# Optimization experiments

Measured on AMD Instinct MI355X. Metric: run time of the kernel, lower is better.

## Reference

```python
import jax, jax.numpy as jnp
import numpy as np

N_EMBED = 1024
N_HEAD = 16
D = N_EMBED // N_HEAD
B, T = 2, 2048
EPS = 1e-5


def _layer_norm(x, w, b):
    mu = jnp.mean(x, axis=-1, keepdims=True)
    var = jnp.mean(jnp.square(x - mu), axis=-1, keepdims=True)
    return (x - mu) * jax.lax.rsqrt(var + EPS) * w + b


def setup_inputs() -> dict:
    key = jax.random.key(0)
    ks = jax.random.split(key, 13)
    E = N_EMBED
    s_attn = 1.0 / np.sqrt(E)
    s_fc = 1.0 / np.sqrt(E)
    s_proj = 1.0 / np.sqrt(4 * E)
    return {
        "x": jax.random.normal(ks[0], (B, T, E), jnp.float32),
        "ln1_w": jnp.ones((E,), jnp.float32),
        "ln1_b": jnp.ones((E,), jnp.float32),
        "w_qkv": jax.random.normal(ks[1], (E, 3 * E), jnp.float32) * s_attn,
        "b_qkv": jax.random.normal(ks[2], (3 * E,), jnp.float32) * 0.02,
        "w_o": jax.random.normal(ks[3], (E, E), jnp.float32) * s_attn,
        "b_o": jax.random.normal(ks[4], (E,), jnp.float32) * 0.02,
        "ln2_w": jnp.ones((E,), jnp.float32),
        "ln2_b": jnp.ones((E,), jnp.float32),
        "w_fc": jax.random.normal(ks[5], (E, 4 * E), jnp.float32) * s_fc,
        "b_fc": jax.random.normal(ks[6], (4 * E,), jnp.float32) * 0.02,
        "w_proj": jax.random.normal(ks[7], (4 * E, E), jnp.float32) * s_proj,
        "b_proj": jax.random.normal(ks[8], (E,), jnp.float32) * 0.02,
    }


def reference(x, ln1_w, ln1_b, w_qkv, b_qkv, w_o, b_o, ln2_w, ln2_b, w_fc, b_fc, w_proj, b_proj):
    Bb, Tt, E = x.shape
    # --- attention branch ---
    h = _layer_norm(x, ln1_w, ln1_b)
    qkv = h @ w_qkv + b_qkv                         # [B,T,3E]
    q, k, v = jnp.split(qkv, 3, axis=-1)
    q = q.reshape(Bb, Tt, N_HEAD, D).transpose(0, 2, 1, 3)  # [B,H,T,D]
    k = k.reshape(Bb, Tt, N_HEAD, D).transpose(0, 2, 1, 3)
    v = v.reshape(Bb, Tt, N_HEAD, D).transpose(0, 2, 1, 3)
    scale = 1.0 / np.sqrt(D)
    a = scale * jnp.einsum("bhqd,bhkd->bhqk", q, k)  # [B,H,T,T]
    causal = jnp.tril(jnp.ones((Tt, Tt), bool))
    a = jnp.where(causal, a, -jnp.inf)
    a = jax.nn.softmax(a, axis=-1)
    y = jnp.einsum("bhqk,bhkd->bhqd", a, v)          # [B,H,T,D]
    y = y.transpose(0, 2, 1, 3).reshape(Bb, Tt, E)
    y = y @ w_o + b_o
    x = x + y
    # --- MLP branch ---
    h = _layer_norm(x, ln2_w, ln2_b)
    h = jax.nn.gelu(h @ w_fc + b_fc, approximate=False)
    h = h @ w_proj + b_proj
    return x + h
```

## Files before the change

### kernel.cpp

```cpp
#include <hip/hip_runtime.h>
#include <cstdint>
#include <cstddef>

#define E 1024
#define TT 2048
#define NB 2
#define NH 16
#define HD 64

using u16 = unsigned short;
using bf16x8 = __attribute__((ext_vector_type(8))) __bf16;
using floatx4 = __attribute__((ext_vector_type(4))) float;
using s16x4 = __attribute__((ext_vector_type(4))) short;

__device__ __forceinline__ float b2f(u16 u) {
  unsigned int x = ((unsigned int)u) << 16;
  float f;
  __builtin_memcpy(&f, &x, 4);
  return f;
}
__device__ __forceinline__ u16 f2b(float f) {
  unsigned int x;
  __builtin_memcpy(&x, &f, 4);
  x += 0x7fffu + ((x >> 16) & 1u);
  return (u16)(x >> 16);
}
__device__ __forceinline__ u16 f2b_fast(float f) {
  unsigned int x;
  float g = f * 1.001953125f;
  __builtin_memcpy(&x, &g, 4);
  return (u16)(x >> 16);
}

__device__ __forceinline__ void async16(const u16* g, u16* l) {
  __builtin_amdgcn_global_load_lds(
      (const __attribute__((address_space(1))) unsigned int*)g,
      (__attribute__((address_space(3))) unsigned int*)l, 16, 0, 0);
}

__device__ __forceinline__ floatx4 mfma32(bf16x8 a, bf16x8 b, floatx4 c) {
  return __builtin_amdgcn_mfma_f32_16x16x32_bf16(a, b, c, 0, 0, 0);
}

__device__ __forceinline__ floatx4 mfma16(s16x4 a, s16x4 b, floatx4 c) {
#if defined(__HIP_DEVICE_COMPILE__)
  return __builtin_amdgcn_mfma_f32_16x16x16bf16_1k(a, b, c, 0, 0, 0);
#else
  return c;
#endif
}

__global__ __launch_bounds__(256) void wconv_all(
    const float* __restrict__ w0, const float* __restrict__ w1,
    const float* __restrict__ w2, const float* __restrict__ w3,
    u16* __restrict__ o0, u16* __restrict__ o1, u16* __restrict__ o2,
    u16* __restrict__ o3) {
  __shared__ float tile[32][33];
  const int t = blockIdx.x;
  const float* w;
  u16* o;
  int K, N, nx, ti;
  if (t < 3072) { w = w0; o = o0; K = 1024; N = 3072; nx = 96; ti = t; }
  else if (t < 4096) { w = w1; o = o1; K = 1024; N = 1024; nx = 32; ti = t - 3072; }
  else if (t < 8192) { w = w2; o = o2; K = 1024; N = 4096; nx = 128; ti = t - 4096; }
  else { w = w3; o = o3; K = 4096; N = 1024; nx = 32; ti = t - 8192; }
  const int n0 = (ti % nx) * 32, k0 = (ti / nx) * 32;
  const int tx = threadIdx.x, ty = threadIdx.y;
#pragma unroll
  for (int i = 0; i < 32; i += 8)
    tile[ty + i][tx] = w[(size_t)(k0 + ty + i) * N + (n0 + tx)];
  __syncthreads();
#pragma unroll
  for (int i = 0; i < 32; i += 8)
    o[(size_t)(n0 + ty + i) * K + (k0 + tx)] = f2b(tile[tx][ty + i]);
}

__global__ __launch_bounds__(256) void ln_kernel(const float* __restrict__ x,
                                                 const float* __restrict__ w,
                                                 const float* __restrict__ bvec,
                                                 u16* __restrict__ outb) {
  const int row = blockIdx.x;
  const int t = threadIdx.x;
  const float4 v = ((const float4*)(x + (size_t)row * E))[t];
  float s1 = v.x + v.y + v.z + v.w;
  float s2 = v.x * v.x + v.y * v.y + v.z * v.z + v.w * v.w;
#pragma unroll
  for (int off = 32; off > 0; off >>= 1) {
    s1 += __shfl_down(s1, off);
    s2 += __shfl_down(s2, off);
  }
  __shared__ float r1[4], r2[4];
  if ((t & 63) == 0) { r1[t >> 6] = s1; r2[t >> 6] = s2; }
  __syncthreads();
  s1 = r1[0] + r1[1] + r1[2] + r1[3];
  s2 = r2[0] + r2[1] + r2[2] + r2[3];
  const float mean = s1 * (1.f / E);
  const float var = s2 * (1.f / E) - mean * mean;
  const float rstd = rsqrtf(var + 1e-5f);
  const float4 wv = ((const float4*)w)[t];
  const float4 bv = ((const float4*)bvec)[t];
  const u16 o0 = f2b((v.x - mean) * rstd * wv.x + bv.x);
  const u16 o1 = f2b((v.y - mean) * rstd * wv.y + bv.y);
  const u16 o2 = f2b((v.z - mean) * rstd * wv.z + bv.z);
  const u16 o3 = f2b((v.w - mean) * rstd * wv.w + bv.w);
  uint2 pk;
  pk.x = (unsigned)o0 | ((unsigned)o1 << 16);
  pk.y = (unsigned)o2 | ((unsigned)o3 << 16);
  ((uint2*)(outb + (size_t)row * E))[t] = pk;
}

template <int MODE, int ROWS>
__global__ __launch_bounds__(512) void gemm_bt(const u16* __restrict__ A,
                                               const u16* __restrict__ BT,
                                               const float* __restrict__ bias,
                                               const float* __restrict__ res,
                                               void* __restrict__ outp,
                                               int M, int N, int K) {
  constexpr int NJ = (ROWS == 256) ? 4 : 2;
  __shared__ __align__(16) u16 As[2][ROWS * 32];
  __shared__ __align__(16) u16 Bs[2][128 * 32];
  const int tid = threadIdx.x;
  const int wave = tid >> 6, lane = tid & 63;

  const int gx = gridDim.x, gy = gridDim.y;
  const int L = blockIdx.y * gx + blockIdx.x;
  const int xc = L & 7, wi = L >> 3;
  const int cpg = gx >> 2;
  const int rpg = gy >> 1;
  const int bxs = (xc >> 1) * cpg + (wi % cpg);
  const int bys = (xc & 1) * rpg + (wi / cpg);

  const int row0 = bys * ROWS, col0 = bxs * 128;
  const int wm = (ROWS == 256) ? (wave & 3) * 64 : (wave & 1) * 64;
  const int wn = (ROWS == 256) ? (wave >> 2) * 64 : (wave >> 1) * 32;
  const int r = lane & 15, qd = lane >> 4;

  floatx4 acc[4][NJ];
#pragma unroll
  for (int i = 0; i < 4; i++)
#pragma unroll
    for (int j = 0; j < NJ; j++) acc[i][j] = (floatx4){0.f, 0.f, 0.f, 0.f};

  const int cA0 = tid, cA1 = tid + 512, cB = tid;
  const u16* ApA = A + (size_t)(row0 + (cA0 >> 2)) * K + (cA0 & 3) * 8;
  const u16* ApB = A + (size_t)(row0 + (cA1 >> 2)) * K + (cA1 & 3) * 8;
  const u16* Bp = BT + (size_t)(col0 + (cB >> 2)) * K + (cB & 3) * 8;

  auto stage = [&](int kt, u16* Asb, u16* Bsb) {
    async16(ApA + kt, Asb + cA0 * 8);
    if (ROWS == 256) async16(ApB + kt, Asb + cA1 * 8);
    async16(Bp + kt, Bsb + cB * 8);
  };
  auto compute = [&](const u16* Asb, const u16* Bsb) {
    bf16x8 af[4], bfr[NJ];
#pragma unroll
    for (int i = 0; i < 4; i++)
      af[i] = *(const bf16x8*)&Asb[(wm + i * 16 + r) * 32 + qd * 8];
#pragma unroll
    for (int j = 0; j < NJ; j++)
      bfr[j] = *(const bf16x8*)&Bsb[(wn + j * 16 + r) * 32 + qd * 8];
#pragma unroll
    for (int i = 0; i < 4; i++)
#pragma unroll
      for (int j = 0; j < NJ; j++)
        acc[i][j] = mfma32(af[i], bfr[j], acc[i][j]);
  };

  const int nIter = K >> 5;
  stage(0, As[0], Bs[0]);
  for (int t = 0; t < nIter; t++) {
    const int tb = t & 1;
    if (t + 1 < nIter) {
      stage((t + 1) * 32, As[tb ^ 1], Bs[tb ^ 1]);
      if (ROWS == 256)
        asm volatile("s_waitcnt vmcnt(3)" ::: "memory");
      else
        asm volatile("s_waitcnt vmcnt(2)" ::: "memory");
    } else {
      asm volatile("s_waitcnt vmcnt(0)" ::: "memory");
    }
    asm volatile("s_barrier" ::: "memory");
    compute(As[tb], Bs[tb]);
    asm volatile("s_barrier" ::: "memory");
  }

#pragma unroll
  for (int i = 0; i < 4; i++) {
#pragma unroll
    for (int j = 0; j < NJ; j++) {
      const int col = col0 + wn + j * 16 + r;
      const float bc = bias[col];
      if (MODE == 3) {
        u16* base = (u16*)outp;
        const int rowb = row0 + wm + i * 16 + qd * 4;
        if (col < 2048) {
          const size_t cb =
              (col < 1024) ? (size_t)col : ((size_t)4096 * 1024 + (col - 1024));
#pragma unroll
          for (int rr = 0; rr < 4; rr++)
            base[cb + (size_t)(rowb + rr) * 1024] = f2b(acc[i][j][rr] + bc);
        } else {
          ushort4 pk;
          pk.x = f2b(acc[i][j][0] + bc);
          pk.y = f2b(acc[i][j][1] + bc);
          pk.z = f2b(acc[i][j][2] + bc);
          pk.w = f2b(acc[i][j][3] + bc);
          *(ushort4*)(base + (size_t)8 * 1024 * 1024 +
                      (size_t)(col - 2048) * 4096 + rowb) = pk;
        }
      } else {
#pragma unroll
        for (int rr = 0; rr < 4; rr++) {
          const int row = row0 + wm + i * 16 + qd * 4 + rr;
          const float v = acc[i][j][rr] + bc;
          const size_t idx = (size_t)row * N + col;
          if (MODE == 0) {
            ((u16*)outp)[idx] = f2b(v);
          } else if (MODE == 1) {
            ((float*)outp)[idx] = v + res[idx];
          } else {
            const float z = 1.5957691216f * v * (1.f + 0.044715f * v * v);
            const float g = v / (1.f + __expf(-z));
            ((u16*)outp)[idx] = f2b(g);
          }
        }
      }
    }
  }
}

__global__ __launch_bounds__(512) void gemm_ks(const u16* __restrict__ A,
                                               const u16* __restrict__ BT,
                                               const float* __restrict__ bias,
                                               const float* __restrict__ res,
                                               float* __restrict__ outp,
                                               int M, int N, int K) {
  __shared__ __align__(16) u16 As[4][2][128 * 32];
  __shared__ __align__(16) u16 Bs[4][2][128 * 32];
  const int tid = threadIdx.x;
  const int wave = tid >> 6, lane = tid & 63;

  const int gx = gridDim.x, gy = gridDim.y;
  const int L = blockIdx.y * gx + blockIdx.x;
  const int xc = L & 7, wi = L >> 3;
  const int cpg = gx >> 2, rpg = gy >> 1;
  const int bxs = (xc >> 1) * cpg + (wi % cpg);
  const int bys = (xc & 1) * rpg + (wi / cpg);

  const int row0 = bys * 128, col0 = bxs * 128;
  const int kg = wave >> 2;
  const int wm = (wave & 1) * 64, wn = ((wave >> 1) & 1) * 64;
  const int r = lane & 15, qd = lane >> 4;

  floatx4 acc[4][4];
#pragma unroll
  for (int i = 0; i < 4; i++)
#pragma unroll
    for (int j = 0; j < 4; j++) acc[i][j] = (floatx4){0.f, 0.f, 0.f, 0.f};

  const int arow = tid >> 2, aslot = (tid & 3) * 8;
  const u16* Ap = A + (size_t)(row0 + arow) * K + aslot;
  const u16* Bp = BT + (size_t)(col0 + arow) * K + aslot;

  auto stage = [&](int s, int d) {
    const int k0 = s * 64;
    async16(Ap + k0, &As[d][0][tid * 8]);
    async16(Ap + k0 + 32, &As[d][1][tid * 8]);
    async16(Bp + k0, &Bs[d][0][tid * 8]);
    async16(Bp + k0 + 32, &Bs[d][1][tid * 8]);
  };
  auto compute = [&](int d) {
    bf16x8 af[4], bfr[4];
#pragma unroll
    for (int i = 0; i < 4; i++)
      af[i] = *(const bf16x8*)&As[d][kg][(wm + i * 16 + r) * 32 + qd * 8];
#pragma unroll
    for (int j = 0; j < 4; j++)
      bfr[j] = *(const bf16x8*)&Bs[d][kg][(wn + j * 16 + r) * 32 + qd * 8];
#pragma unroll
    for (int i = 0; i < 4; i++)
#pragma unroll
      for (int j = 0; j < 4; j++)
        acc[i][j] = mfma32(af[i], bfr[j], acc[i][j]);
  };

  const int nT = K >> 6;
  stage(0, 0);
  stage(1, 1);
  stage(2, 2);
  for (int tt = 0; tt < nT; tt += 4) {
#pragma unroll
    for (int d = 0; d < 4; d++) {
      const int t = tt + d;
      const int rem = nT - 1 - t;
      if (rem >= 2)
        asm volatile("s_waitcnt vmcnt(8)" ::: "memory");
      else if (rem == 1)
        asm volatile("s_waitcnt vmcnt(4)" ::: "memory");
      else
        asm volatile("s_waitcnt vmcnt(0)" ::: "memory");
      asm volatile("s_barrier" ::: "memory");
      if (t + 3 < nT) stage(t + 3, (d + 3) & 3);
      compute(d);
    }
  }

  __syncthreads();
  float* S = (float*)&As[0][0][0];
  const int p = wave & 3;
  floatx4* W = (floatx4*)S + p * 1024 + lane;
  if (kg == 1) {
#pragma unroll
    for (int i = 0; i < 4; i++)
#pragma unroll
      for (int j = 0; j < 4; j++) W[(i * 4 + j) * 64] = acc[i][j];
  }
  __syncthreads();
  if (kg == 0) {
#pragma unroll
    for (int i = 0; i < 4; i++) {
#pragma unroll
      for (int j = 0; j < 4; j++) {
        const floatx4 w2 = W[(i * 4 + j) * 64];
        const int col = col0 + wn + j * 16 + r;
        const float bc = bias[col];
#pragma unroll
        for (int rr = 0; rr < 4; rr++) {
          const int row = row0 + wm + i * 16 + qd * 4 + rr;
          const size_t idx = (size_t)row * N + col;
          outp[idx] = acc[i][j][rr] + w2[rr] + bc + res[idx];
        }
      }
    }
  }
}

__global__ __launch_bounds__(256, 2) void attn_mfma(const u16* __restrict__ qb,
                                                    const u16* __restrict__ kb,
                                                    const u16* __restrict__ vtb,
                                                    u16* __restrict__ y) {
  const int bx = blockIdx.x;
  const int h = blockIdx.y, b = blockIdx.z;
  const int qt = b ? (15 - bx) : bx;
  const int tid = threadIdx.x;
  const int wave = tid >> 6, lane = tid & 63;
  const int quad = lane >> 4, r = lane & 15;

  __shared__ __align__(16) u16 Ks[2][128 * 64];
  __shared__ __align__(16) u16 Vs[2][64 * 128];

  const float C = 0.125f * 1.44269504f;
  const int qbase = qt * 128 + wave * 32;

  bf16x8 qf[2][2];
#pragma unroll
  for (int f = 0; f < 2; f++) {
    const u16* qp = qb + ((size_t)b * TT + qbase + f * 16 + r) * E + h * 64;
#pragma unroll
    for (int kh = 0; kh < 2; kh++) {
      union { bf16x8 v; u16 u[8]; } tmp;
#pragma unroll
      for (int j = 0; j < 8; j++) tmp.u[j] = f2b(b2f(qp[kh * 32 + quad * 8 + j]) * C);
      qf[f][kh] = tmp.v;
    }
  }

  floatx4 o[2][4];
#pragma unroll
  for (int f = 0; f < 2; f++)
#pragma unroll
    for (int i = 0; i < 4; i++) o[f][i] = (floatx4){0.f, 0.f, 0.f, 0.f};
  float lsum[2] = {0.f, 0.f};
  const bool mgt[4] = {(quad * 4 + 0) > r, (quad * 4 + 1) > r,
                       (quad * 4 + 2) > r, (quad * 4 + 3) > r};

  auto stageKV = [&](int it, int bi) {
    const int k0 = it * 128;
#pragma unroll
    for (int i = 0; i < 4; i++) {
      const int c = tid + i * 256;
      const int key = c >> 3, dc = (c & 7) ^ (key & 7);
      async16(kb + ((size_t)b * TT + k0 + key) * E + h * 64 + dc * 8, &Ks[bi][c * 8]);
    }
#pragma unroll
    for (int i = 0; i < 4; i++) {
      const int c = tid + i * 256;
      const int d = c >> 4, kc = (c & 15) ^ (d & 15);
      async16(vtb + (size_t)(h * 64 + d) * (NB * TT) + b * TT + k0 + kc * 8,
              &Vs[bi][c * 8]);
    }
  };

  const int nIter = qt + 1;
  stageKV(0, 0);
  for (int it = 0; it < nIter; it++) {
    if (it + 1 < nIter) {
      stageKV(it + 1, (it + 1) & 1);
      asm volatile("s_waitcnt vmcnt(8)" ::: "memory");
    } else {
      asm volatile("s_waitcnt vmcnt(0)" ::: "memory");
    }
    asm volatile("s_barrier" ::: "memory");
    const u16* Kb = Ks[it & 1];
    const u16* Vb = Vs[it & 1];
    const int k0 = it * 128;
    const int relA = (qbase - k0) >> 4;
    const int kTop = (relA + 1 < 7) ? (relA + 1) : 7;

    floatx4 s[2][8];
#pragma unroll
    for (int ks = 0; ks < 8; ks++) {
      if (ks <= kTop) {
        const int key = ks * 16 + r, kx = key & 7;
        const bf16x8 kf0 = *(const bf16x8*)&Kb[key * 64 + (quad ^ kx) * 8];
        const bf16x8 kf1 = *(const bf16x8*)&Kb[key * 64 + ((4 + quad) ^ kx) * 8];
        floatx4 a0 = (floatx4){0.f, 0.f, 0.f, 0.f};
        a0 = mfma32(kf0, qf[0][0], a0);
        a0 = mfma32(kf1, qf[0][1], a0);
        s[0][ks] = a0;
        floatx4 a1 = (floatx4){0.f, 0.f, 0.f, 0.f};
        a1 = mfma32(kf0, qf[1][0], a1);
        a1 = mfma32(kf1, qf[1][1], a1);
        s[1][ks] = a1;
      }
    }

#pragma unroll
    for (int ks = 0; ks < 8; ks++) {
      if (ks <= kTop) {
        s16x4 vf[4];
#pragma unroll
        for (int dsub = 0; dsub < 4; dsub++) {
          const int d = dsub * 16 + r;
          vf[dsub] = *(const s16x4*)&Vb[d * 128 + ((2 * ks + (quad >> 1)) ^ r) * 8 +
                                        (quad & 1) * 4];
        }
#pragma unroll
        for (int f = 0; f < 2; f++) {
          const int rel = relA + f;
          if (ks <= rel) {
            float p0 = exp2f(s[f][ks][0]);
            float p1 = exp2f(s[f][ks][1]);
            float p2 = exp2f(s[f][ks][2]);
            float p3 = exp2f(s[f][ks][3]);
            if (ks == rel) {
              if (mgt[0]) p0 = 0.f;
              if (mgt[1]) p1 = 0.f;
              if (mgt[2]) p2 = 0.f;
              if (mgt[3]) p3 = 0.f;
            }
            lsum[f] += p0 + p1 + p2 + p3;
            s16x4 pk;
            pk[0] = (short)f2b_fast(p0);
            pk[1] = (short)f2b_fast(p1);
            pk[2] = (short)f2b_fast(p2);
            pk[3] = (short)f2b_fast(p3);
#pragma unroll
            for (int dsub = 0; dsub < 4; dsub++)
              o[f][dsub] = mfma16(pk, vf[dsub], o[f][dsub]);
          }
        }
      }
    }
    asm volatile("s_barrier" ::: "memory");
  }

#pragma unroll
  for (int f = 0; f < 2; f++) {
    float lv = lsum[f];
    lv += __shfl_xor(lv, 16);
    lv += __shfl_xor(lv, 32);
#pragma unroll
    for (int rr = 0; rr < 4; rr++) {
      const float linv = 1.f / __shfl(lv, quad * 4 + rr);
      const size_t row = (size_t)b * TT + qbase + f * 16 + quad * 4 + rr;
#pragma unroll
      for (int dsub = 0; dsub < 4; dsub++)
        y[row * E + h * 64 + dsub * 16 + r] = f2b(o[f][dsub][rr] * linv);
    }
  }
}

extern "C" void kernel_launch(void* const* d_in, const int* in_sizes, int n_in,
                              void* d_out, int out_size, void* d_ws, size_t ws_size,
                              hipStream_t stream) {
  (void)in_sizes; (void)n_in; (void)out_size; (void)ws_size;
  const float* x      = (const float*)d_in[0];
  const float* ln1w   = (const float*)d_in[1];
  const float* ln1b   = (const float*)d_in[2];
  const float* w_qkv  = (const float*)d_in[3];
  const float* b_qkv  = (const float*)d_in[4];
  const float* w_o    = (const float*)d_in[5];
  const float* b_o    = (const float*)d_in[6];
  const float* ln2w   = (const float*)d_in[7];
  const float* ln2b   = (const float*)d_in[8];
  const float* w_fc   = (const float*)d_in[9];
  const float* b_fc   = (const float*)d_in[10];
  const float* w_proj = (const float*)d_in[11];
  const float* b_proj = (const float*)d_in[12];
  float* out = (float*)d_out;

  char* p = (char*)d_ws;
  u16* wT_qkv  = (u16*)p; p += (size_t)3072 * 1024 * 2;
  u16* wT_o    = (u16*)p; p += (size_t)1024 * 1024 * 2;
  u16* wT_fc   = (u16*)p; p += (size_t)4096 * 1024 * 2;
  u16* wT_proj = (u16*)p; p += (size_t)1024 * 4096 * 2;
  u16* hbuf    = (u16*)p; p += (size_t)4096 * 1024 * 2;
  u16* qkvb    = (u16*)p; p += (size_t)4096 * 3072 * 2;
  float* x2    = (float*)p; p += (size_t)4096 * 1024 * 4;
  u16* gbuf    = (u16*)p; p += (size_t)4096 * 4096 * 2;

  u16* qb  = qkvb;
  u16* kb  = qkvb + (size_t)4096 * 1024;
  u16* vtb = qkvb + (size_t)8 * 1024 * 1024;

  wconv_all<<<12288, dim3(32, 8), 0, stream>>>(w_qkv, w_o, w_fc, w_proj,
                                               wT_qkv, wT_o, wT_fc, wT_proj);

  ln_kernel<<<4096, 256, 0, stream>>>(x, ln1w, ln1b, hbuf);
  gemm_bt<3, 256><<<dim3(3072 / 128, 4096 / 256), 512, 0, stream>>>(
      hbuf, wT_qkv, b_qkv, nullptr, qkvb, 4096, 3072, 1024);
  attn_mfma<<<dim3(16, NH, NB), 256, 0, stream>>>(qb, kb, vtb, hbuf);
  gemm_ks<<<dim3(1024 / 128, 4096 / 128), 512, 0, stream>>>(
      hbuf, wT_o, b_o, x, x2, 4096, 1024, 1024);
  ln_kernel<<<4096, 256, 0, stream>>>(x2, ln2w, ln2b, hbuf);
  gemm_bt<2, 256><<<dim3(4096 / 128, 4096 / 256), 512, 0, stream>>>(
      hbuf, wT_fc, b_fc, nullptr, gbuf, 4096, 4096, 1024);
  gemm_ks<<<dim3(1024 / 128, 4096 / 128), 512, 0, stream>>>(
      gbuf, wT_proj, b_proj, x2, out, 4096, 1024, 4096);
}
```

Measured before the change: 341.1 us.

## Split attention key tiles across two wave groups and reduce through LDS

Doubles the attention block to 512 threads. Each query slice is handled by two waves, and each wave processes half of the 128-key tile. The partial outputs and row sums are combined through shared memory at the end. This aims to raise occupancy and halve per-wave serial work, at the cost of an extra LDS reduction, a barrier, and more idle waves on causal diagonal tiles.

```diff
diff --git a/kernel.cpp b/kernel.cpp
--- a/kernel.cpp
+++ b/kernel.cpp
@@ -335,7 +335,7 @@
   }
 }
 
-__global__ __launch_bounds__(256, 2) void attn_mfma(const u16* __restrict__ qb,
+__global__ __launch_bounds__(512, 4) void attn_mfma(const u16* __restrict__ qb,
                                                     const u16* __restrict__ kb,
                                                     const u16* __restrict__ vtb,
                                                     u16* __restrict__ y) {
@@ -345,12 +345,15 @@
   const int tid = threadIdx.x;
   const int wave = tid >> 6, lane = tid & 63;
   const int quad = lane >> 4, r = lane & 15;
-
-  __shared__ __align__(16) u16 Ks[2][128 * 64];
-  __shared__ __align__(16) u16 Vs[2][64 * 128];
+  const int wq = wave & 3;
+  const int kvh = wave >> 2;
+
+  __shared__ __align__(16) u16 lds[2 * 128 * 64 + 2 * 64 * 128];
+  u16* KsB = lds;
+  u16* VsB = lds + 2 * 128 * 64;
 
   const float C = 0.125f * 1.44269504f;
-  const int qbase = qt * 128 + wave * 32;
+  const int qbase = qt * 128 + wq * 32;
 
   bf16x8 qf[2][2];
 #pragma unroll
@@ -376,18 +379,20 @@
 
   auto stageKV = [&](int it, int bi) {
     const int k0 = it * 128;
-#pragma unroll
-    for (int i = 0; i < 4; i++) {
-      const int c = tid + i * 256;
+    u16* Kd = KsB + bi * (128 * 64);
+    u16* Vd = VsB + bi * (64 * 128);
+#pragma unroll
+    for (int i = 0; i < 2; i++) {
+      const int c = tid + i * 512;
       const int key = c >> 3, dc = (c & 7) ^ (key & 7);
-      async16(kb + ((size_t)b * TT + k0 + key) * E + h * 64 + dc * 8, &Ks[bi][c * 8]);
-    }
-#pragma unroll
-    for (int i = 0; i < 4; i++) {
-      const int c = tid + i * 256;
+      async16(kb + ((size_t)b * TT + k0 + key) * E + h * 64 + dc * 8, Kd + c * 8);
+    }
+#pragma unroll
+    for (int i = 0; i < 2; i++) {
+      const int c = tid + i * 512;
       const int d = c >> 4, kc = (c & 15) ^ (d & 15);
       async16(vtb + (size_t)(h * 64 + d) * (NB * TT) + b * TT + k0 + kc * 8,
-              &Vs[bi][c * 8]);
+              Vd + c * 8);
     }
   };
 
@@ -396,38 +401,31 @@
   for (int it = 0; it < nIter; it++) {
     if (it + 1 < nIter) {
       stageKV(it + 1, (it + 1) & 1);
-      asm volatile("s_waitcnt vmcnt(8)" ::: "memory");
+      asm volatile("s_waitcnt vmcnt(4)" ::: "memory");
     } else {
       asm volatile("s_waitcnt vmcnt(0)" ::: "memory");
     }
     asm volatile("s_barrier" ::: "memory");
-    const u16* Kb = Ks[it & 1];
-    const u16* Vb = Vs[it & 1];
+    const u16* Kb = KsB + (it & 1) * (128 * 64);
+    const u16* Vb = VsB + (it & 1) * (64 * 128);
     const int k0 = it * 128;
     const int relA = (qbase - k0) >> 4;
     const int kTop = (relA + 1 < 7) ? (relA + 1) : 7;
 
-    floatx4 s[2][8];
-#pragma unroll
-    for (int ks = 0; ks < 8; ks++) {
+#pragma unroll
+    for (int kk = 0; kk < 4; kk++) {
+      const int ks = kvh * 4 + kk;
       if (ks <= kTop) {
         const int key = ks * 16 + r, kx = key & 7;
         const bf16x8 kf0 = *(const bf16x8*)&Kb[key * 64 + (quad ^ kx) * 8];
         const bf16x8 kf1 = *(const bf16x8*)&Kb[key * 64 + ((4 + quad) ^ kx) * 8];
-        floatx4 a0 = (floatx4){0.f, 0.f, 0.f, 0.f};
-        a0 = mfma32(kf0, qf[0][0], a0);
-        a0 = mfma32(kf1, qf[0][1], a0);
-        s[0][ks] = a0;
-        floatx4 a1 = (floatx4){0.f, 0.f, 0.f, 0.f};
-        a1 = mfma32(kf0, qf[1][0], a1);
-        a1 = mfma32(kf1, qf[1][1], a1);
-        s[1][ks] = a1;
-      }
-    }
-
-#pragma unroll
-    for (int ks = 0; ks < 8; ks++) {
-      if (ks <= kTop) {
+        floatx4 s0 = (floatx4){0.f, 0.f, 0.f, 0.f};
+        s0 = mfma32(kf0, qf[0][0], s0);
+        s0 = mfma32(kf1, qf[0][1], s0);
+        floatx4 s1 = (floatx4){0.f, 0.f, 0.f, 0.f};
+        s1 = mfma32(kf0, qf[1][0], s1);
+        s1 = mfma32(kf1, qf[1][1], s1);
+
         s16x4 vf[4];
 #pragma unroll
         for (int dsub = 0; dsub < 4; dsub++) {
@@ -435,14 +433,16 @@
           vf[dsub] = *(const s16x4*)&Vb[d * 128 + ((2 * ks + (quad >> 1)) ^ r) * 8 +
                                         (quad & 1) * 4];
         }
+
 #pragma unroll
         for (int f = 0; f < 2; f++) {
+          const floatx4 sv = (f == 0) ? s0 : s1;
           const int rel = relA + f;
           if (ks <= rel) {
-            float p0 = exp2f(s[f][ks][0]);
-            float p1 = exp2f(s[f][ks][1]);
-            float p2 = exp2f(s[f][ks][2]);
-            float p3 = exp2f(s[f][ks][3]);
+            float p0 = exp2f(sv[0]);
+            float p1 = exp2f(sv[1]);
+            float p2 = exp2f(sv[2]);
+            float p3 = exp2f(sv[3]);
             if (ks == rel) {
               if (mgt[0]) p0 = 0.f;
               if (mgt[1]) p1 = 0.f;
@@ -465,18 +465,35 @@
     asm volatile("s_barrier" ::: "memory");
   }
 
-#pragma unroll
-  for (int f = 0; f < 2; f++) {
-    float lv = lsum[f];
-    lv += __shfl_xor(lv, 16);
-    lv += __shfl_xor(lv, 32);
-#pragma unroll
-    for (int rr = 0; rr < 4; rr++) {
-      const float linv = 1.f / __shfl(lv, quad * 4 + rr);
-      const size_t row = (size_t)b * TT + qbase + f * 16 + quad * 4 + rr;
-#pragma unroll
-      for (int dsub = 0; dsub < 4; dsub++)
-        y[row * E + h * 64 + dsub * 16 + r] = f2b(o[f][dsub][rr] * linv);
+  floatx4* W = (floatx4*)(float*)lds + wq * 576 + lane;
+  if (kvh == 1) {
+#pragma unroll
+    for (int f = 0; f < 2; f++)
+#pragma unroll
+      for (int dsub = 0; dsub < 4; dsub++) W[(f * 4 + dsub) * 64] = o[f][dsub];
+    W[8 * 64] = (floatx4){lsum[0], lsum[1], 0.f, 0.f};
+  }
+  __syncthreads();
+  if (kvh == 0) {
+    const floatx4 ls2 = W[8 * 64];
+#pragma unroll
+    for (int f = 0; f < 2; f++) {
+      float lv = lsum[f] + ((f == 0) ? ls2[0] : ls2[1]);
+      lv += __shfl_xor(lv, 16);
+      lv += __shfl_xor(lv, 32);
+      float linv[4];
+#pragma unroll
+      for (int rr = 0; rr < 4; rr++) linv[rr] = 1.f / __shfl(lv, quad * 4 + rr);
+#pragma unroll
+      for (int dsub = 0; dsub < 4; dsub++) {
+        const floatx4 o2 = W[(f * 4 + dsub) * 64];
+#pragma unroll
+        for (int rr = 0; rr < 4; rr++) {
+          const size_t row = (size_t)b * TT + qbase + f * 16 + quad * 4 + rr;
+          y[row * E + h * 64 + dsub * 16 + r] =
+              f2b((o[f][dsub][rr] + o2[rr]) * linv[rr]);
+        }
+      }
     }
   }
 }
@@ -520,7 +537,7 @@
   ln_kernel<<<4096, 256, 0, stream>>>(x, ln1w, ln1b, hbuf);
   gemm_bt<3, 256><<<dim3(3072 / 128, 4096 / 256), 512, 0, stream>>>(
       hbuf, wT_qkv, b_qkv, nullptr, qkvb, 4096, 3072, 1024);
-  attn_mfma<<<dim3(16, NH, NB), 256, 0, stream>>>(qb, kb, vtb, hbuf);
+  attn_mfma<<<dim3(16, NH, NB), 512, 0, stream>>>(qb, kb, vtb, hbuf);
   gemm_ks<<<dim3(1024 / 128, 4096 / 128), 512, 0, stream>>>(
       hbuf, wT_o, b_o, x, x2, 4096, 1024, 1024);
   ln_kernel<<<4096, 256, 0, stream>>>(x2, ln2w, ln2b, hbuf);
```

Result: faster. 319.1 us (-6.4%).
